# Optimization experiments

Hardware: AMD Instinct MI355X
Metric: run time of the kernel (lower is better)

## Reference

```python
import jax, jax.numpy as jnp
import numpy as np

K = 3
PAD = K // 2


def setup_inputs() -> dict:
    key = jax.random.key(0)
    k1, k2 = jax.random.split(key)
    B, C, H, W = 8, 32, 256, 256
    x = jax.random.normal(k1, (B, C, H, W), dtype=jnp.float32)
    dynamic_filters = jax.random.normal(k2, (B, C * K * K, H, W), dtype=jnp.float32)
    return {"x": x, "dynamic_filters": dynamic_filters}


def _dynamic_filter(x, dynamic_filters):
    B, C, H, W = x.shape
    # Pad spatially (zero pad, matching F.unfold padding)
    xp = jnp.pad(x, ((0, 0), (0, 0), (PAD, PAD), (PAD, PAD)))
    # Filters laid out as view(B, C, K*K, H, W): offsets row-major (i, j)
    f = dynamic_filters.reshape(B, C, K * K, H, W)
    out = jnp.zeros((B, C, H, W), dtype=x.dtype)
    # Small fixed K^2 = 9 loop: gather shifted window, multiply-accumulate.
    # Avoids materializing the full [B, C, K^2, H, W] unfolded buffer at once
    # in eager mode; XLA fuses this into a single pass.
    for i in range(K):
        for j in range(K):
            out = out + xp[:, :, i:i + H, j:j + W] * f[:, :, i * K + j]
    return out


def reference(x, dynamic_filters):
    return _dynamic_filter(x, dynamic_filters)
```

## Files before the change

kernel.cpp:

```cpp
#include <hip/hip_runtime.h>


constexpr int Bc = 8;
constexpr int Cc = 32;
constexpr int Hc = 256;
constexpr int Wc = 256;
constexpr int HW = Hc * Wc;
constexpr int W4 = Wc / 4;

__global__ __launch_bounds__(256) void dyn_filter_kernel(
    const float* __restrict__ x,
    const float* __restrict__ f,
    float* __restrict__ out)
{
    int idx = blockIdx.x * blockDim.x + threadIdx.x;
    if (idx >= Bc * Cc * Hc * W4) return;

    int w4 = idx & (W4 - 1);
    int t  = idx >> 6;
    int h  = t & (Hc - 1);
    int bc = t >> 8;
    int w0 = w4 << 2;

    const float* xplane = x + (size_t)bc * HW;
    const float* fbase  = f + (size_t)bc * 9 * HW + (size_t)h * Wc + w0;

    float4 acc = make_float4(0.f, 0.f, 0.f, 0.f);

#pragma unroll
    for (int di = 0; di < 3; ++di) {
        int hy = h + di - 1;
        if (hy < 0 || hy >= Hc) continue;
        const float* xrow = xplane + (size_t)hy * Wc + w0;
        float4 mid  = *(const float4*)(xrow);
        float  left  = (w0 > 0)      ? xrow[-1] : 0.f;
        float  right = (w0 + 4 < Wc) ? xrow[4]  : 0.f;

        {
            float4 ff = *(const float4*)(fbase + (size_t)(di * 3 + 0) * HW);
            acc.x += left  * ff.x;
            acc.y += mid.x * ff.y;
            acc.z += mid.y * ff.z;
            acc.w += mid.z * ff.w;
        }
        {
            float4 ff = *(const float4*)(fbase + (size_t)(di * 3 + 1) * HW);
            acc.x += mid.x * ff.x;
            acc.y += mid.y * ff.y;
            acc.z += mid.z * ff.z;
            acc.w += mid.w * ff.w;
        }
        {
            float4 ff = *(const float4*)(fbase + (size_t)(di * 3 + 2) * HW);
            acc.x += mid.y * ff.x;
            acc.y += mid.z * ff.y;
            acc.z += mid.w * ff.z;
            acc.w += right * ff.w;
        }
    }

    *(float4*)(out + (size_t)bc * HW + (size_t)h * Wc + w0) = acc;
}

extern "C" void kernel_launch(void* const* d_in, const int* in_sizes, int n_in,
                              void* d_out, int out_size, void* d_ws, size_t ws_size,
                              hipStream_t stream) {
    const float* x = (const float*)d_in[0];
    const float* f = (const float*)d_in[1];
    float* out = (float*)d_out;

    int total = Bc * Cc * Hc * W4;
    int block = 256;
    int grid  = (total + block - 1) / block;
    dyn_filter_kernel<<<grid, block, 0, stream>>>(x, f, out);
}
```

Measured before the change: 806.0 us.

## Compute two output rows per thread with wavefront shuffles for halos

```diff
diff --git a/kernel.cpp b/kernel.cpp
--- a/kernel.cpp
+++ b/kernel.cpp
@@ -1,5 +1,7 @@
 #include <hip/hip_runtime.h>
 
+
+typedef float v4f __attribute__((ext_vector_type(4)));
 
 constexpr int Bc = 8;
 constexpr int Cc = 32;
@@ -7,59 +9,79 @@
 constexpr int Wc = 256;
 constexpr int HW = Hc * Wc;
 constexpr int W4 = Wc / 4;
+constexpr int H2 = Hc / 2;
 
 __global__ __launch_bounds__(256) void dyn_filter_kernel(
     const float* __restrict__ x,
     const float* __restrict__ f,
     float* __restrict__ out)
 {
-    int idx = blockIdx.x * blockDim.x + threadIdx.x;
-    if (idx >= Bc * Cc * Hc * W4) return;
+    int idx  = blockIdx.x * blockDim.x + threadIdx.x;
+    int lane = threadIdx.x & 63;
 
     int w4 = idx & (W4 - 1);
     int t  = idx >> 6;
-    int h  = t & (Hc - 1);
-    int bc = t >> 8;
+    int hh = t & (H2 - 1);
+    int bc = t >> 7;
+    int h0 = hh << 1;
     int w0 = w4 << 2;
 
-    const float* xplane = x + (size_t)bc * HW;
-    const float* fbase  = f + (size_t)bc * 9 * HW + (size_t)h * Wc + w0;
+    const float* xrowbase = x + (size_t)bc * HW + w0;
+    v4f r[4];
+#pragma unroll
+    for (int k = 0; k < 4; ++k) {
+        int hy = h0 - 1 + k;
+        if (hy >= 0 && hy < Hc)
+            r[k] = *(const v4f*)(xrowbase + (size_t)hy * Wc);
+        else
+            r[k] = (v4f)(0.f);
+    }
 
-    float4 acc = make_float4(0.f, 0.f, 0.f, 0.f);
+    float lft[4], rgt[4];
+#pragma unroll
+    for (int k = 0; k < 4; ++k) {
+        lft[k] = __shfl_up(r[k].w, 1);
+        rgt[k] = __shfl_down(r[k].x, 1);
+        if (lane == 0)  lft[k] = 0.f;
+        if (lane == 63) rgt[k] = 0.f;
+    }
+
+    const float* fbase = f + (size_t)bc * 9 * HW + (size_t)h0 * Wc + w0;
+
+    v4f a0 = (v4f)(0.f);
+    v4f a1 = (v4f)(0.f);
 
 #pragma unroll
     for (int di = 0; di < 3; ++di) {
-        int hy = h + di - 1;
-        if (hy < 0 || hy >= Hc) continue;
-        const float* xrow = xplane + (size_t)hy * Wc + w0;
-        float4 mid  = *(const float4*)(xrow);
-        float  left  = (w0 > 0)      ? xrow[-1] : 0.f;
-        float  right = (w0 + 4 < Wc) ? xrow[4]  : 0.f;
+        v4f   xa = r[di];
+        v4f   xb = r[di + 1];
+        float la = lft[di],     lb = lft[di + 1];
+        float ra = rgt[di],     rb = rgt[di + 1];
+#pragma unroll
+        for (int dj = 0; dj < 3; ++dj) {
+            const float* fp = fbase + (size_t)(di * 3 + dj) * HW;
+            v4f f0 = __builtin_nontemporal_load((const v4f*)fp);
+            v4f f1 = __builtin_nontemporal_load((const v4f*)(fp + Wc));
 
-        {
-            float4 ff = *(const float4*)(fbase + (size_t)(di * 3 + 0) * HW);
-            acc.x += left  * ff.x;
-            acc.y += mid.x * ff.y;
-            acc.z += mid.y * ff.z;
-            acc.w += mid.z * ff.w;
-        }
-        {
-            float4 ff = *(const float4*)(fbase + (size_t)(di * 3 + 1) * HW);
-            acc.x += mid.x * ff.x;
-            acc.y += mid.y * ff.y;
-            acc.z += mid.z * ff.z;
-            acc.w += mid.w * ff.w;
-        }
-        {
-            float4 ff = *(const float4*)(fbase + (size_t)(di * 3 + 2) * HW);
-            acc.x += mid.y * ff.x;
-            acc.y += mid.z * ff.y;
-            acc.z += mid.w * ff.z;
-            acc.w += right * ff.w;
+            v4f wa, wb;
+            if (dj == 0) {
+                wa = (v4f){la,   xa.x, xa.y, xa.z};
+                wb = (v4f){lb,   xb.x, xb.y, xb.z};
+            } else if (dj == 1) {
+                wa = xa;
+                wb = xb;
+            } else {
+                wa = (v4f){xa.y, xa.z, xa.w, ra};
+                wb = (v4f){xb.y, xb.z, xb.w, rb};
+            }
+            a0 += wa * f0;
+            a1 += wb * f1;
         }
     }
 
-    *(float4*)(out + (size_t)bc * HW + (size_t)h * Wc + w0) = acc;
+    float* op = out + (size_t)bc * HW + (size_t)h0 * Wc + w0;
+    __builtin_nontemporal_store(a0, (v4f*)op);
+    __builtin_nontemporal_store(a1, (v4f*)(op + Wc));
 }
 
 extern "C" void kernel_launch(void* const* d_in, const int* in_sizes, int n_in,
@@ -69,7 +91,7 @@
     const float* f = (const float*)d_in[1];
     float* out = (float*)d_out;
 
-    int total = Bc * Cc * Hc * W4;
+    int total = Bc * Cc * H2 * W4;
     int block = 256;
     int grid  = (total + block - 1) / block;
     dyn_filter_kernel<<<grid, block, 0, stream>>>(x, f, out);
```

Measured after the change: 789.8 us. 1.02x faster.
